# Optimization experiments

Hardware: AMD Instinct MI355X
Metric: run time of the kernel (lower is better)

The kernel has to match this reference:

```python
import jax, jax.numpy as jnp
import numpy as np

N = 50000        # nodes
E = 1_600_000    # edges
D_IN = 128       # input_dim
H = 2            # n_heads
C = 32           # out_dim per head


def setup_inputs() -> dict:
    key = jax.random.key(0)
    ks = jax.random.split(key, 10)
    x = jax.random.normal(ks[0], (N, D_IN), dtype=jnp.float32)
    edge_index = jax.random.randint(ks[1], (2, E), 0, N, dtype=jnp.int64)
    s = 1.0 / np.sqrt(D_IN)
    Wq = jax.random.uniform(ks[2], (D_IN, H * C), jnp.float32, -s, s)
    bq = jax.random.uniform(ks[3], (H * C,), jnp.float32, -s, s)
    Wk = jax.random.uniform(ks[4], (D_IN, H * C), jnp.float32, -s, s)
    bk = jax.random.uniform(ks[5], (H * C,), jnp.float32, -s, s)
    Wv = jax.random.uniform(ks[6], (D_IN, H * C), jnp.float32, -s, s)
    bv = jax.random.uniform(ks[7], (H * C,), jnp.float32, -s, s)
    Wskip = jax.random.uniform(ks[8], (D_IN, H * C), jnp.float32, -s, s)
    bskip = jax.random.uniform(ks[9], (H * C,), jnp.float32, -s, s)
    return {"x": x, "edge_index": edge_index, "Wq": Wq, "bq": bq,
            "Wk": Wk, "bk": bk, "Wv": Wv, "bv": bv,
            "Wskip": Wskip, "bskip": bskip}


def reference(x, edge_index, Wq, bq, Wk, bk, Wv, bv, Wskip, bskip):
    # IntraGraphAttention.forward: ELU then TransformerConv (PyG semantics,
    # concat=True, root_weight=True, beta=False).
    x = jax.nn.elu(x)
    src, dst = edge_index[0], edge_index[1]

    q = (x @ Wq + bq).reshape(N, H, C)   # queries at target nodes
    k = (x @ Wk + bk).reshape(N, H, C)   # keys at source nodes
    v = (x @ Wv + bv).reshape(N, H, C)   # values at source nodes

    # per-edge attention logits [E, H]
    alpha = jnp.einsum('ehc,ehc->eh', q[dst], k[src]) / np.sqrt(C).astype(np.float32)

    # segment softmax over incoming edges of each target node
    m = jax.ops.segment_max(alpha, dst, num_segments=N)            # [N, H]
    m = jnp.where(jnp.isfinite(m), m, 0.0)                          # empty segments
    ex = jnp.exp(alpha - m[dst])                                    # [E, H]
    denom = jax.ops.segment_sum(ex, dst, num_segments=N)            # [N, H]
    w = ex / jnp.maximum(denom[dst], 1e-16)                         # [E, H]

    # weighted scatter-add of values to targets
    msg = v[src] * w[:, :, None]                                    # [E, H, C]
    out = jax.ops.segment_sum(msg, dst, num_segments=N)             # [N, H, C]
    out = out.reshape(N, H * C)

    # root/skip connection
    return out + x @ Wskip + bskip
```

## Files before the change

kernel.cpp:

```cpp
#include <hip/hip_runtime.h>
#include <hip/hip_bf16.h>


#define DIN 128
#define HC  64
#define EPB 4096
#define CAPB 12288
#define CAPQ 3072

typedef _Float16 h2 __attribute__((ext_vector_type(2)));
typedef _Float16 h4 __attribute__((ext_vector_type(4)));
typedef _Float16 h8 __attribute__((ext_vector_type(8)));
typedef float    f4 __attribute__((ext_vector_type(4)));
typedef float    f2v __attribute__((ext_vector_type(2)));

#if defined(__has_builtin)
#if __has_builtin(__builtin_amdgcn_fdot2)
#define HAVE_FDOT2 1
#endif
#endif

static __device__ __forceinline__ float fdot2(h2 a, h2 b, float c) {
#ifdef HAVE_FDOT2
    return __builtin_amdgcn_fdot2(a, b, c, false);
#else
    return fmaf((float)a.x, (float)b.x, fmaf((float)a.y, (float)b.y, c));
#endif
}

__global__ __launch_bounds__(256) void k_prep(
        const float* __restrict__ Wq, const float* __restrict__ Wk,
        const float* __restrict__ Wv, const float* __restrict__ Ws,
        _Float16* __restrict__ Wh, int* __restrict__ bucketCnt) {
    int t = threadIdx.x;
    if (blockIdx.x == 0) bucketCnt[t] = 0;
    int idx = blockIdx.x * 256 + t;
    int m    = idx >> 13;
    int rem  = idx & 8191;
    int grp  = rem >> 9;
    int ks   = grp >> 2;
    int nt   = grp & 3;
    int r3   = rem & 511;
    int lane = r3 >> 3;
    int j    = r3 & 7;
    int k = ks * 32 + (lane >> 4) * 8 + j;
    int n = nt * 16 + (lane & 15);
    const float* W = (m == 0) ? Wq : (m == 1) ? Wk : (m == 2) ? Wv : Ws;
    Wh[idx] = (_Float16)W[k * 64 + n];
}

#define TB 32
#define XS 136
__global__ __launch_bounds__(256) void k_fused(
        const float4* __restrict__ x4,
        const _Float16* __restrict__ Wh,
        const float* __restrict__ bq, const float* __restrict__ bk,
        const float* __restrict__ bv, const float* __restrict__ bs,
        _Float16* __restrict__ Q, unsigned char* __restrict__ KV8,
        float* __restrict__ OUT, int N,
        const int* __restrict__ ei, int* __restrict__ bucketCnt,
        unsigned int* __restrict__ part, int E, int cb) {
    __shared__ alignas(16) char smem[4096 + EPB * 4];
    int t = threadIdx.x;

    if ((int)blockIdx.x < cb) {
        int* hist  = (int*)smem;
        int* lbase = hist + 256;
        int* gbase = lbase + 256;
        int* wsum  = gbase + 256;
        unsigned int* stg = (unsigned int*)(smem + 4096);

        int e0 = (int)blockIdx.x * EPB;
        int cnt = min(EPB, E - e0);
        hist[t] = 0;
        __syncthreads();

        unsigned int pk[EPB / 256];
        unsigned short rk[EPB / 256];
        #pragma unroll
        for (int u = 0; u < EPB / 256; ++u) {
            int i = t + u * 256;
            if (i < cnt) {
                unsigned int d = (unsigned int)ei[E + e0 + i];
                unsigned int s = (unsigned int)ei[e0 + i];
                pk[u] = (d << 16) | s;
                rk[u] = (unsigned short)atomicAdd(&hist[d >> 8], 1);
            }
        }
        __syncthreads();

        int lane = t & 63, wid = t >> 6;
        int v = hist[t];
        int x = v;
        #pragma unroll
        for (int off = 1; off < 64; off <<= 1) {
            int y = __shfl_up(x, off, 64);
            if (lane >= off) x += y;
        }
        if (lane == 63) wsum[wid] = x;
        __syncthreads();
        int wpre = 0;
        #pragma unroll
        for (int w = 0; w < 4; ++w) wpre += (w < wid) ? wsum[w] : 0;
        lbase[t] = wpre + x - v;
        if (v > 0) {
            int base = atomicAdd(&bucketCnt[t], v);
            base = min(base, CAPB - v);
            gbase[t] = t * CAPB + base;
        }
        __syncthreads();

        #pragma unroll
        for (int u = 0; u < EPB / 256; ++u) {
            int i = t + u * 256;
            if (i < cnt) stg[lbase[pk[u] >> 24] + (int)rk[u]] = pk[u];
        }
        __syncthreads();
        for (int i = t; i < cnt; i += 256) {
            unsigned int pkv = stg[i];
            int b = pkv >> 24;
            part[gbase[b] + (i - lbase[b])] = pkv;
        }
        return;
    }

    _Float16* xs = (_Float16*)smem;
    int n0 = ((int)blockIdx.x - cb) * TB;

    #pragma unroll
    for (int u = 0; u < 4; ++u) {
        int idx = t + u * 256;
        int row = idx >> 5;
        int k4  = idx & 31;
        int node = n0 + row;
        float4 v = make_float4(0.f, 0.f, 0.f, 0.f);
        if (node < N) v = x4[(size_t)node * 32 + k4];
        v.x = (v.x > 0.f) ? v.x : (__expf(v.x) - 1.0f);
        v.y = (v.y > 0.f) ? v.y : (__expf(v.y) - 1.0f);
        v.z = (v.z > 0.f) ? v.z : (__expf(v.z) - 1.0f);
        v.w = (v.w > 0.f) ? v.w : (__expf(v.w) - 1.0f);
        h4 hv = { (_Float16)v.x, (_Float16)v.y, (_Float16)v.z, (_Float16)v.w };
        *(h4*)&xs[row * XS + k4 * 4] = hv;
    }
    __syncthreads();

    int m    = t >> 6;
    int lane = t & 63;
    int lr   = lane & 15;
    int lq   = lane >> 4;

    const _Float16* Wm = Wh + m * 8192;
    const float* bias = (m == 0) ? bq : (m == 1) ? bk : (m == 2) ? bv : bs;

    f4 acc[2][4];
    #pragma unroll
    for (int mt = 0; mt < 2; ++mt)
        #pragma unroll
        for (int nt = 0; nt < 4; ++nt)
            acc[mt][nt] = (f4){0.f, 0.f, 0.f, 0.f};

    #pragma unroll
    for (int ks = 0; ks < 4; ++ks) {
        h8 a0 = *(const h8*)&xs[lr * XS + ks * 32 + lq * 8];
        h8 a1 = *(const h8*)&xs[(16 + lr) * XS + ks * 32 + lq * 8];
        #pragma unroll
        for (int nt = 0; nt < 4; ++nt) {
            h8 b = *(const h8*)&Wm[((ks * 4 + nt) << 9) + lane * 8];
            acc[0][nt] = __builtin_amdgcn_mfma_f32_16x16x32_f16(a0, b, acc[0][nt], 0, 0, 0);
            acc[1][nt] = __builtin_amdgcn_mfma_f32_16x16x32_f16(a1, b, acc[1][nt], 0, 0, 0);
        }
    }

    #pragma unroll
    for (int nt = 0; nt < 4; ++nt) {
        int col = nt * 16 + lr;
        float bb = bias[col];
        #pragma unroll
        for (int mt = 0; mt < 2; ++mt) {
            #pragma unroll
            for (int r = 0; r < 4; ++r) {
                int node = n0 + mt * 16 + lq * 4 + r;
                if (node < N) {
                    float val = acc[mt][nt][r] + bb;
                    if (m == 3) {
                        OUT[((size_t)node << 6) + col] = val;
                    } else if (m == 0) {
                        Q[((size_t)node << 6) + col] = (_Float16)val;
                    } else {
                        int pk8 = __builtin_amdgcn_cvt_pk_fp8_f32(val, val, 0, false);
                        KV8[((size_t)node << 7) + ((m == 2) ? 64 : 0) + col] =
                            (unsigned char)(pk8 & 0xFF);
                    }
                }
            }
        }
    }
}

__global__ __launch_bounds__(512) void k_build(
        const unsigned int* __restrict__ part, const int* __restrict__ bucketCnt,
        unsigned short* __restrict__ srcs16, int* __restrict__ row_ptr,
        int N, int NBK, int E) {
    __shared__ int hist[256], basep[256], cur[64], sd[256];
    __shared__ unsigned short sbuf[CAPQ];
    __shared__ int s_outBase, s_cnt;
    int t = threadIdx.x;
    int bqid = blockIdx.x;
    int b = bqid >> 2;
    int h = bqid & 3;

    int bc = (t < NBK) ? bucketCnt[t] : 0;
    if (t < 256) sd[t] = bc;
    __syncthreads();
    for (int off = 1; off < 256; off <<= 1) {
        int xv = (t >= off && t < 256) ? sd[t - off] : 0;
        __syncthreads();
        if (t < 256) sd[t] += xv;
        __syncthreads();
    }
    if (t == b) { s_outBase = sd[t] - bc; s_cnt = bc; }
    if (bqid == 0 && t == 256) row_ptr[N] = E;
    if (t < 256) hist[t] = 0;
    if (t < 64) cur[t] = 0;
    __syncthreads();
    int outBase = s_outBase;
    int cnt = min(s_cnt, CAPB);
    int s0 = b * CAPB;

    for (int i = t; i < cnt; i += 512) {
        atomicAdd(&hist[(part[s0 + i] >> 16) & 255], 1);
    }
    __syncthreads();
    {
        int v = (t < 256) ? hist[t] : 0;
        if (t < 256) sd[t] = v;
        __syncthreads();
        for (int off = 1; off < 256; off <<= 1) {
            int xv = (t >= off && t < 256) ? sd[t - off] : 0;
            __syncthreads();
            if (t < 256) sd[t] += xv;
            __syncthreads();
        }
        if (t < 256) basep[t] = sd[t] - v;
    }
    __syncthreads();

    int lo = h << 6;
    int base0 = basep[lo];
    int qcnt = ((h == 3) ? cnt : basep[lo + 64]) - base0;

    for (int i = t; i < cnt; i += 512) {
        unsigned int pkv = part[s0 + i];
        int d = (pkv >> 16) & 255;
        if ((d >> 6) == h) {
            int r = atomicAdd(&cur[d - lo], 1);
            int pos = basep[d] - base0 + r;
            if (pos < CAPQ) sbuf[pos] = (unsigned short)(pkv & 0xFFFFu);
        }
    }
    __syncthreads();
    for (int i = t; i < qcnt && i < CAPQ; i += 512)
        srcs16[outBase + base0 + i] = sbuf[i];

    int node = (b << 8) + lo + t;
    if (t < 64 && node < N) row_ptr[node] = outBase + basep[lo + t];
}

__global__ __launch_bounds__(256) void k_attn(
        const _Float16* __restrict__ Q, const unsigned char* __restrict__ KV8,
        const int* __restrict__ row_ptr,
        const unsigned short* __restrict__ srcs16, float* __restrict__ out, int N) {
    int lane = threadIdx.x & 63;
    int wave = threadIdx.x >> 6;
    int n = blockIdx.x * 4 + wave;
    if (n >= N) return;
    int h5 = lane & 32;
    int c  = lane & 31;
    int eg = (lane >> 3) & 3;
    int ch = lane & 7;

    int start = row_ptr[n];
    int deg   = row_ptr[n + 1] - start;
    if (deg <= 0) return;

    h8 q8[4];
    {
        const h8* qp = (const h8*)(Q + ((size_t)n << 6) + h5);
        #pragma unroll
        for (int r = 0; r < 4; ++r) q8[r] = qp[r];
    }
    const h2* q2 = (const h2*)q8;

    const float scale = 0.17677669529663687f;
    float lsum = 0.f;
    f4 acc = (f4){0.f, 0.f, 0.f, 0.f};

    unsigned vofs = 64u + (unsigned)h5 + ((unsigned)ch << 2);

    int sc_cur = (c < deg) ? (int)srcs16[start + c] : 0;
    uint4 ka, kb;
    {
        unsigned ko = ((unsigned)sc_cur << 7) + (unsigned)h5;
        ka = *(const uint4*)(KV8 + ko);
        kb = *(const uint4*)(KV8 + ko + 16);
    }

    for (int i0 = 0; i0 < deg; i0 += 32) {
        int nb = min(32, deg - i0);
        int sc = sc_cur;
        int i1 = i0 + 32;

        int sc_next = 0;
        if (i1 < deg && c < deg - i1) sc_next = (int)srcs16[start + i1 + c];

        float s0 = 0.f, s1 = 0.f, s2 = 0.f, s3 = 0.f;
#define KDOT(kw, idx, ss) { \
        f2v f01 = __builtin_amdgcn_cvt_pk_f32_fp8((int)(kw), false); \
        f2v f23 = __builtin_amdgcn_cvt_pk_f32_fp8((int)(kw), true);  \
        auto p01 = __builtin_amdgcn_cvt_pkrtz(f01[0], f01[1]); \
        auto p23 = __builtin_amdgcn_cvt_pkrtz(f23[0], f23[1]); \
        ss = fdot2(*(h2*)&p01, q2[2*(idx)],   ss); \
        ss = fdot2(*(h2*)&p23, q2[2*(idx)+1], ss); }
        KDOT(ka.x, 0, s0) KDOT(ka.y, 1, s1) KDOT(ka.z, 2, s2) KDOT(ka.w, 3, s3)
        KDOT(kb.x, 4, s0) KDOT(kb.y, 5, s1) KDOT(kb.z, 6, s2) KDOT(kb.w, 7, s3)
#undef KDOT
        float s = (s0 + s1) + (s2 + s3);
        float ex = (c < nb) ? __expf(s * scale) : 0.f;
        lsum += ex;

        if (i1 < deg) {
            unsigned ko = ((unsigned)sc_next << 7) + (unsigned)h5;
            ka = *(const uint4*)(KV8 + ko);
            kb = *(const uint4*)(KV8 + ko + 16);
        }
        sc_cur = sc_next;

        float wv[8]; int sj[8];
        #pragma unroll
        for (int u = 0; u < 8; ++u) {
            int j = 4 * u + eg;
            wv[u] = __shfl(ex, h5 + j, 64);
            sj[u] = __shfl(sc, h5 + j, 64);
        }
        unsigned vw[8];
        #pragma unroll
        for (int u = 0; u < 8; ++u)
            vw[u] = *(const unsigned int*)(KV8 + (((unsigned)sj[u] << 7) + vofs));
        #pragma unroll
        for (int u = 0; u < 8; ++u) {
            f2v v01 = __builtin_amdgcn_cvt_pk_f32_fp8((int)vw[u], false);
            f2v v23 = __builtin_amdgcn_cvt_pk_f32_fp8((int)vw[u], true);
            acc[0] = fmaf(wv[u], v01[0], acc[0]);
            acc[1] = fmaf(wv[u], v01[1], acc[1]);
            acc[2] = fmaf(wv[u], v23[0], acc[2]);
            acc[3] = fmaf(wv[u], v23[1], acc[3]);
        }
    }

    #pragma unroll
    for (int i = 0; i < 4; ++i) {
        acc[i] += __shfl_xor(acc[i], 8, 64);
        acc[i] += __shfl_xor(acc[i], 16, 64);
    }

    float ls = lsum;
    ls += __shfl_xor(ls, 16, 64);
    ls += __shfl_xor(ls,  8, 64);
    ls += __shfl_xor(ls,  4, 64);
    ls += __shfl_xor(ls,  2, 64);
    ls += __shfl_xor(ls,  1, 64);
    float rden = 1.0f / fmaxf(ls, 1e-16f);

    if ((lane & 24) == 0) {
        float4* o4 = (float4*)out + ((size_t)n << 4) + (h5 >> 2) + ch;
        float4 cur4 = *o4;
        cur4.x += acc[0] * rden;
        cur4.y += acc[1] * rden;
        cur4.z += acc[2] * rden;
        cur4.w += acc[3] * rden;
        *o4 = cur4;
    }
}

extern "C" void kernel_launch(void* const* d_in, const int* in_sizes, int n_in,
                              void* d_out, int out_size, void* d_ws, size_t ws_size,
                              hipStream_t stream) {
    const float* x  = (const float*)d_in[0];
    const int*   ei = (const int*)d_in[1];
    const float* Wq = (const float*)d_in[2];
    const float* bq = (const float*)d_in[3];
    const float* Wk = (const float*)d_in[4];
    const float* bk = (const float*)d_in[5];
    const float* Wv = (const float*)d_in[6];
    const float* bv = (const float*)d_in[7];
    const float* Ws = (const float*)d_in[8];
    const float* bs = (const float*)d_in[9];
    float* out = (float*)d_out;

    int N = in_sizes[0] / DIN;
    int E = in_sizes[1] / 2;
    int NBK = (N + 255) >> 8;

    char* ws = (char*)d_ws;
    size_t off = 0;
    auto carve = [&](size_t bytes) -> void* {
        void* p = ws + off;
        off = (off + bytes + 255) & ~(size_t)255;
        return p;
    };
    int*            bucketCnt = (int*)carve(256 * sizeof(int));
    int*            row_ptr   = (int*)carve((size_t)(N + 1) * sizeof(int));
    unsigned int*   part      = (unsigned int*)carve((size_t)NBK * CAPB * sizeof(unsigned int));
    unsigned short* srcs16    = (unsigned short*)carve((size_t)E * sizeof(unsigned short));
    _Float16*       Wh        = (_Float16*)carve(4 * 8192 * sizeof(_Float16));
    _Float16*       Qh        = (_Float16*)carve((size_t)N * HC * sizeof(_Float16));
    unsigned char*  KV8       = (unsigned char*)carve((size_t)N * 128);
    (void)ws_size; (void)n_in; (void)out_size;

    int qb = (N + TB - 1) / TB;
    int cb = (E + EPB - 1) / EPB;

    k_prep<<<128, 256, 0, stream>>>(Wq, Wk, Wv, Ws, Wh, bucketCnt);
    k_fused<<<qb + cb, 256, 0, stream>>>(
        (const float4*)x, Wh, bq, bk, bv, bs,
        Qh, KV8, out, N,
        ei, bucketCnt, part, E, cb);
    k_build<<<4 * NBK, 512, 0, stream>>>(part, bucketCnt, srcs16, row_ptr, N, NBK, E);
    k_attn<<<(N + 3) / 4, 256, 0, stream>>>(Qh, KV8, row_ptr, srcs16, out, N);
}
```

Before: 172.7 us.

## Replace bucketed two-pass CSR build with global degree histogram, scan, atomic scatter

Swaps the two-level radix partition (per-block LDS bucketing into a fixed-capacity staging buffer, then a per-bucket build kernel) for a counting-sort CSR build. A global per-node degree histogram is built with atomics, a two-kernel prefix scan produces row_ptr and cursors, and a scatter pass places each source via a global atomicAdd on its destination cursor. This drops the capacity-clamped partition buffer and the build kernel. In exchange it adds a memset, two extra launches, an extra read of the edge list, and 1.6M contended global atomics with random 2-byte writes. Neighbor order within a row becomes nondeterministic.

```diff
diff --git a/kernel.cpp b/kernel.cpp
--- a/kernel.cpp
+++ b/kernel.cpp
@@ -4,9 +4,6 @@
 
 #define DIN 128
 #define HC  64
-#define EPB 4096
-#define CAPB 12288
-#define CAPQ 3072
 
 typedef _Float16 h2 __attribute__((ext_vector_type(2)));
 typedef _Float16 h4 __attribute__((ext_vector_type(4)));
@@ -31,22 +28,80 @@
 __global__ __launch_bounds__(256) void k_prep(
         const float* __restrict__ Wq, const float* __restrict__ Wk,
         const float* __restrict__ Wv, const float* __restrict__ Ws,
-        _Float16* __restrict__ Wh, int* __restrict__ bucketCnt) {
+        _Float16* __restrict__ Wh,
+        const int* __restrict__ ei, int* __restrict__ deg, int E) {
     int t = threadIdx.x;
-    if (blockIdx.x == 0) bucketCnt[t] = 0;
-    int idx = blockIdx.x * 256 + t;
-    int m    = idx >> 13;
-    int rem  = idx & 8191;
-    int grp  = rem >> 9;
-    int ks   = grp >> 2;
-    int nt   = grp & 3;
-    int r3   = rem & 511;
-    int lane = r3 >> 3;
-    int j    = r3 & 7;
-    int k = ks * 32 + (lane >> 4) * 8 + j;
-    int n = nt * 16 + (lane & 15);
-    const float* W = (m == 0) ? Wq : (m == 1) ? Wk : (m == 2) ? Wv : Ws;
-    Wh[idx] = (_Float16)W[k * 64 + n];
+    if ((int)blockIdx.x < 128) {
+        int idx = blockIdx.x * 256 + t;
+        int m    = idx >> 13;
+        int rem  = idx & 8191;
+        int grp  = rem >> 9;
+        int ks   = grp >> 2;
+        int nt   = grp & 3;
+        int r3   = rem & 511;
+        int lane = r3 >> 3;
+        int j    = r3 & 7;
+        int k = ks * 32 + (lane >> 4) * 8 + j;
+        int n = nt * 16 + (lane & 15);
+        const float* W = (m == 0) ? Wq : (m == 1) ? Wk : (m == 2) ? Wv : Ws;
+        Wh[idx] = (_Float16)W[k * 64 + n];
+        return;
+    }
+    int base = ((int)blockIdx.x - 128) * 1024;
+    #pragma unroll
+    for (int u = 0; u < 4; ++u) {
+        int i = base + u * 256 + t;
+        if (i < E) atomicAdd(&deg[ei[E + i]], 1);
+    }
+}
+
+__global__ __launch_bounds__(256) void k_scanA(
+        const int* __restrict__ deg, int* __restrict__ chunkSum, int N) {
+    int t = threadIdx.x;
+    int node = (int)blockIdx.x * 256 + t;
+    int v = (node < N) ? deg[node] : 0;
+    #pragma unroll
+    for (int off = 1; off < 64; off <<= 1) v += __shfl_xor(v, off, 64);
+    __shared__ int ws[4];
+    if ((t & 63) == 0) ws[t >> 6] = v;
+    __syncthreads();
+    if (t == 0) chunkSum[blockIdx.x] = ws[0] + ws[1] + ws[2] + ws[3];
+}
+
+__global__ __launch_bounds__(256) void k_scanB(
+        const int* __restrict__ deg, const int* __restrict__ chunkSum,
+        int* __restrict__ row_ptr, int* __restrict__ cur, int N, int E) {
+    __shared__ int ws[4], sbase[1];
+    int t = threadIdx.x, j = (int)blockIdx.x;
+    int lane = t & 63, wid = t >> 6;
+
+    int c = (t < j) ? chunkSum[t] : 0;
+    int cr = c;
+    #pragma unroll
+    for (int off = 1; off < 64; off <<= 1) cr += __shfl_xor(cr, off, 64);
+    if (lane == 0) ws[wid] = cr;
+    __syncthreads();
+    if (t == 0) sbase[0] = ws[0] + ws[1] + ws[2] + ws[3];
+    __syncthreads();
+    int base = sbase[0];
+    __syncthreads();
+
+    int node = j * 256 + t;
+    int v = (node < N) ? deg[node] : 0;
+    int x = v;
+    #pragma unroll
+    for (int off = 1; off < 64; off <<= 1) {
+        int y = __shfl_up(x, off, 64);
+        if (lane >= off) x += y;
+    }
+    if (lane == 63) ws[wid] = x;
+    __syncthreads();
+    int wpre = 0;
+    #pragma unroll
+    for (int w = 0; w < 4; ++w) wpre += (w < wid) ? ws[w] : 0;
+    int excl = base + wpre + x - v;
+    if (node < N) { row_ptr[node] = excl; cur[node] = excl; }
+    if (j == 0 && t == 0) row_ptr[N] = E;
 }
 
 #define TB 32
@@ -58,74 +113,27 @@
         const float* __restrict__ bv, const float* __restrict__ bs,
         _Float16* __restrict__ Q, unsigned char* __restrict__ KV8,
         float* __restrict__ OUT, int N,
-        const int* __restrict__ ei, int* __restrict__ bucketCnt,
-        unsigned int* __restrict__ part, int E, int cb) {
-    __shared__ alignas(16) char smem[4096 + EPB * 4];
+        const int* __restrict__ ei, int* __restrict__ cur,
+        unsigned short* __restrict__ srcs16, int E, int qb) {
+    __shared__ alignas(16) _Float16 xs[32 * XS];
     int t = threadIdx.x;
 
-    if ((int)blockIdx.x < cb) {
-        int* hist  = (int*)smem;
-        int* lbase = hist + 256;
-        int* gbase = lbase + 256;
-        int* wsum  = gbase + 256;
-        unsigned int* stg = (unsigned int*)(smem + 4096);
-
-        int e0 = (int)blockIdx.x * EPB;
-        int cnt = min(EPB, E - e0);
-        hist[t] = 0;
-        __syncthreads();
-
-        unsigned int pk[EPB / 256];
-        unsigned short rk[EPB / 256];
-        #pragma unroll
-        for (int u = 0; u < EPB / 256; ++u) {
-            int i = t + u * 256;
-            if (i < cnt) {
-                unsigned int d = (unsigned int)ei[E + e0 + i];
-                unsigned int s = (unsigned int)ei[e0 + i];
-                pk[u] = (d << 16) | s;
-                rk[u] = (unsigned short)atomicAdd(&hist[d >> 8], 1);
+    if ((int)blockIdx.x >= qb) {
+        int base = ((int)blockIdx.x - qb) * 1024;
+        #pragma unroll
+        for (int u = 0; u < 4; ++u) {
+            int i = base + u * 256 + t;
+            if (i < E) {
+                int s = ei[i];
+                int d = ei[E + i];
+                int pos = atomicAdd(&cur[d], 1);
+                srcs16[pos] = (unsigned short)s;
             }
         }
-        __syncthreads();
-
-        int lane = t & 63, wid = t >> 6;
-        int v = hist[t];
-        int x = v;
-        #pragma unroll
-        for (int off = 1; off < 64; off <<= 1) {
-            int y = __shfl_up(x, off, 64);
-            if (lane >= off) x += y;
-        }
-        if (lane == 63) wsum[wid] = x;
-        __syncthreads();
-        int wpre = 0;
-        #pragma unroll
-        for (int w = 0; w < 4; ++w) wpre += (w < wid) ? wsum[w] : 0;
-        lbase[t] = wpre + x - v;
-        if (v > 0) {
-            int base = atomicAdd(&bucketCnt[t], v);
-            base = min(base, CAPB - v);
-            gbase[t] = t * CAPB + base;
-        }
-        __syncthreads();
-
-        #pragma unroll
-        for (int u = 0; u < EPB / 256; ++u) {
-            int i = t + u * 256;
-            if (i < cnt) stg[lbase[pk[u] >> 24] + (int)rk[u]] = pk[u];
-        }
-        __syncthreads();
-        for (int i = t; i < cnt; i += 256) {
-            unsigned int pkv = stg[i];
-            int b = pkv >> 24;
-            part[gbase[b] + (i - lbase[b])] = pkv;
-        }
         return;
     }
 
-    _Float16* xs = (_Float16*)smem;
-    int n0 = ((int)blockIdx.x - cb) * TB;
+    int n0 = (int)blockIdx.x * TB;
 
     #pragma unroll
     for (int u = 0; u < 4; ++u) {
@@ -197,75 +205,6 @@
     }
 }
 
-__global__ __launch_bounds__(512) void k_build(
-        const unsigned int* __restrict__ part, const int* __restrict__ bucketCnt,
-        unsigned short* __restrict__ srcs16, int* __restrict__ row_ptr,
-        int N, int NBK, int E) {
-    __shared__ int hist[256], basep[256], cur[64], sd[256];
-    __shared__ unsigned short sbuf[CAPQ];
-    __shared__ int s_outBase, s_cnt;
-    int t = threadIdx.x;
-    int bqid = blockIdx.x;
-    int b = bqid >> 2;
-    int h = bqid & 3;
-
-    int bc = (t < NBK) ? bucketCnt[t] : 0;
-    if (t < 256) sd[t] = bc;
-    __syncthreads();
-    for (int off = 1; off < 256; off <<= 1) {
-        int xv = (t >= off && t < 256) ? sd[t - off] : 0;
-        __syncthreads();
-        if (t < 256) sd[t] += xv;
-        __syncthreads();
-    }
-    if (t == b) { s_outBase = sd[t] - bc; s_cnt = bc; }
-    if (bqid == 0 && t == 256) row_ptr[N] = E;
-    if (t < 256) hist[t] = 0;
-    if (t < 64) cur[t] = 0;
-    __syncthreads();
-    int outBase = s_outBase;
-    int cnt = min(s_cnt, CAPB);
-    int s0 = b * CAPB;
-
-    for (int i = t; i < cnt; i += 512) {
-        atomicAdd(&hist[(part[s0 + i] >> 16) & 255], 1);
-    }
-    __syncthreads();
-    {
-        int v = (t < 256) ? hist[t] : 0;
-        if (t < 256) sd[t] = v;
-        __syncthreads();
-        for (int off = 1; off < 256; off <<= 1) {
-            int xv = (t >= off && t < 256) ? sd[t - off] : 0;
-            __syncthreads();
-            if (t < 256) sd[t] += xv;
-            __syncthreads();
-        }
-        if (t < 256) basep[t] = sd[t] - v;
-    }
-    __syncthreads();
-
-    int lo = h << 6;
-    int base0 = basep[lo];
-    int qcnt = ((h == 3) ? cnt : basep[lo + 64]) - base0;
-
-    for (int i = t; i < cnt; i += 512) {
-        unsigned int pkv = part[s0 + i];
-        int d = (pkv >> 16) & 255;
-        if ((d >> 6) == h) {
-            int r = atomicAdd(&cur[d - lo], 1);
-            int pos = basep[d] - base0 + r;
-            if (pos < CAPQ) sbuf[pos] = (unsigned short)(pkv & 0xFFFFu);
-        }
-    }
-    __syncthreads();
-    for (int i = t; i < qcnt && i < CAPQ; i += 512)
-        srcs16[outBase + base0 + i] = sbuf[i];
-
-    int node = (b << 8) + lo + t;
-    if (t < 64 && node < N) row_ptr[node] = outBase + basep[lo + t];
-}
-
 __global__ __launch_bounds__(256) void k_attn(
         const _Float16* __restrict__ Q, const unsigned char* __restrict__ KV8,
         const int* __restrict__ row_ptr,
@@ -408,9 +347,10 @@
         off = (off + bytes + 255) & ~(size_t)255;
         return p;
     };
-    int*            bucketCnt = (int*)carve(256 * sizeof(int));
+    int*            deg       = (int*)carve((size_t)N * sizeof(int));
+    int*            cur       = (int*)carve((size_t)N * sizeof(int));
     int*            row_ptr   = (int*)carve((size_t)(N + 1) * sizeof(int));
-    unsigned int*   part      = (unsigned int*)carve((size_t)NBK * CAPB * sizeof(unsigned int));
+    int*            chunkSum  = (int*)carve((size_t)NBK * sizeof(int));
     unsigned short* srcs16    = (unsigned short*)carve((size_t)E * sizeof(unsigned short));
     _Float16*       Wh        = (_Float16*)carve(4 * 8192 * sizeof(_Float16));
     _Float16*       Qh        = (_Float16*)carve((size_t)N * HC * sizeof(_Float16));
@@ -418,13 +358,15 @@
     (void)ws_size; (void)n_in; (void)out_size;
 
     int qb = (N + TB - 1) / TB;
-    int cb = (E + EPB - 1) / EPB;
-
-    k_prep<<<128, 256, 0, stream>>>(Wq, Wk, Wv, Ws, Wh, bucketCnt);
-    k_fused<<<qb + cb, 256, 0, stream>>>(
+    int eb = (E + 1023) / 1024;
+
+    hipMemsetAsync(deg, 0, (size_t)N * sizeof(int), stream);
+    k_prep<<<128 + eb, 256, 0, stream>>>(Wq, Wk, Wv, Ws, Wh, ei, deg, E);
+    k_scanA<<<NBK, 256, 0, stream>>>(deg, chunkSum, N);
+    k_scanB<<<NBK, 256, 0, stream>>>(deg, chunkSum, row_ptr, cur, N, E);
+    k_fused<<<qb + eb, 256, 0, stream>>>(
         (const float4*)x, Wh, bq, bk, bv, bs,
         Qh, KV8, out, N,
-        ei, bucketCnt, part, E, cb);
-    k_build<<<4 * NBK, 512, 0, stream>>>(part, bucketCnt, srcs16, row_ptr, N, NBK, E);
+        ei, cur, srcs16, E, qb);
     k_attn<<<(N + 3) / 4, 256, 0, stream>>>(Qh, KV8, row_ptr, srcs16, out, N);
 }
```

After: 344.3 us. +99.3%, slower.

## Rewrite CSR build as one 1024-thread block per bucket with register-held ranks

Applied to the files above, without the earlier changes.

The CSR build kernel now runs one 1024-thread block per 256-node bucket instead of four 512-thread blocks per bucket that each handled a quarter of the destinations. Each thread reads its partition entries once into registers, takes its local rank from the histogram atomic, and scatters using the exclusive scan, so the second global read and the per-quarter cursor atomics are gone. Both scans use wave shuffles instead of a barrier-heavy shared-memory loop. The cost is fewer blocks in flight, a larger shared buffer and more registers per thread, which may limit occupancy.

```diff
diff --git a/kernel.cpp b/kernel.cpp
--- a/kernel.cpp
+++ b/kernel.cpp
@@ -6,7 +6,6 @@
 #define HC  64
 #define EPB 4096
 #define CAPB 12288
-#define CAPQ 3072
 
 typedef _Float16 h2 __attribute__((ext_vector_type(2)));
 typedef _Float16 h4 __attribute__((ext_vector_type(4)));
@@ -197,73 +196,82 @@
     }
 }
 
-__global__ __launch_bounds__(512) void k_build(
+__global__ __launch_bounds__(1024) void k_build(
         const unsigned int* __restrict__ part, const int* __restrict__ bucketCnt,
         unsigned short* __restrict__ srcs16, int* __restrict__ row_ptr,
         int N, int NBK, int E) {
-    __shared__ int hist[256], basep[256], cur[64], sd[256];
-    __shared__ unsigned short sbuf[CAPQ];
+    __shared__ int hist[256], basep[256], wsum[4], sums[4];
+    __shared__ unsigned short sbuf[CAPB];
     __shared__ int s_outBase, s_cnt;
     int t = threadIdx.x;
-    int bqid = blockIdx.x;
-    int b = bqid >> 2;
-    int h = bqid & 3;
-
-    int bc = (t < NBK) ? bucketCnt[t] : 0;
-    if (t < 256) sd[t] = bc;
-    __syncthreads();
-    for (int off = 1; off < 256; off <<= 1) {
-        int xv = (t >= off && t < 256) ? sd[t - off] : 0;
-        __syncthreads();
-        if (t < 256) sd[t] += xv;
-        __syncthreads();
-    }
-    if (t == b) { s_outBase = sd[t] - bc; s_cnt = bc; }
-    if (bqid == 0 && t == 256) row_ptr[N] = E;
-    if (t < 256) hist[t] = 0;
-    if (t < 64) cur[t] = 0;
-    __syncthreads();
+    int b = blockIdx.x;
+    int lane = t & 63, wid = t >> 6;
+
+    if (t < 256) {
+        hist[t] = 0;
+        int c = (t < NBK && t < b) ? bucketCnt[t] : 0;
+        #pragma unroll
+        for (int off = 1; off < 64; off <<= 1) c += __shfl_xor(c, off, 64);
+        if (lane == 0) sums[wid] = c;
+    }
+    if (t == 1023) s_cnt = min(bucketCnt[b], CAPB);
+    __syncthreads();
+    if (t == 0) s_outBase = sums[0] + sums[1] + sums[2] + sums[3];
+    __syncthreads();
+    int cnt = s_cnt;
     int outBase = s_outBase;
-    int cnt = min(s_cnt, CAPB);
     int s0 = b * CAPB;
 
-    for (int i = t; i < cnt; i += 512) {
-        atomicAdd(&hist[(part[s0 + i] >> 16) & 255], 1);
-    }
-    __syncthreads();
-    {
-        int v = (t < 256) ? hist[t] : 0;
-        if (t < 256) sd[t] = v;
-        __syncthreads();
-        for (int off = 1; off < 256; off <<= 1) {
-            int xv = (t >= off && t < 256) ? sd[t - off] : 0;
-            __syncthreads();
-            if (t < 256) sd[t] += xv;
-            __syncthreads();
-        }
-        if (t < 256) basep[t] = sd[t] - v;
-    }
-    __syncthreads();
-
-    int lo = h << 6;
-    int base0 = basep[lo];
-    int qcnt = ((h == 3) ? cnt : basep[lo + 64]) - base0;
-
-    for (int i = t; i < cnt; i += 512) {
-        unsigned int pkv = part[s0 + i];
-        int d = (pkv >> 16) & 255;
-        if ((d >> 6) == h) {
-            int r = atomicAdd(&cur[d - lo], 1);
-            int pos = basep[d] - base0 + r;
-            if (pos < CAPQ) sbuf[pos] = (unsigned short)(pkv & 0xFFFFu);
-        }
-    }
-    __syncthreads();
-    for (int i = t; i < qcnt && i < CAPQ; i += 512)
-        srcs16[outBase + base0 + i] = sbuf[i];
-
-    int node = (b << 8) + lo + t;
-    if (t < 64 && node < N) row_ptr[node] = outBase + basep[lo + t];
+    unsigned int pk[CAPB / 1024];
+    int rk[CAPB / 1024];
+    #pragma unroll
+    for (int u = 0; u < CAPB / 1024; ++u) {
+        int i = t + u * 1024;
+        if (i < cnt) {
+            pk[u] = part[s0 + i];
+            rk[u] = atomicAdd(&hist[(pk[u] >> 16) & 255], 1);
+        }
+    }
+    __syncthreads();
+
+    if (t < 256) {
+        int v = hist[t];
+        int x = v;
+        #pragma unroll
+        for (int off = 1; off < 64; off <<= 1) {
+            int y = __shfl_up(x, off, 64);
+            if (lane >= off) x += y;
+        }
+        if (lane == 63) wsum[wid] = x;
+        basep[t] = x - v;
+    }
+    __syncthreads();
+    if (t < 256) {
+        int wpre = 0;
+        #pragma unroll
+        for (int w = 0; w < 4; ++w) wpre += (w < wid) ? wsum[w] : 0;
+        basep[t] += wpre;
+    }
+    __syncthreads();
+
+    #pragma unroll
+    for (int u = 0; u < CAPB / 1024; ++u) {
+        int i = t + u * 1024;
+        if (i < cnt) {
+            int d = (pk[u] >> 16) & 255;
+            int pos = basep[d] + rk[u];
+            if (pos < CAPB) sbuf[pos] = (unsigned short)(pk[u] & 0xFFFFu);
+        }
+    }
+    __syncthreads();
+
+    for (int i = t; i < cnt; i += 1024)
+        srcs16[outBase + i] = sbuf[i];
+    if (t < 256) {
+        int node = (b << 8) + t;
+        if (node < N) row_ptr[node] = outBase + basep[t];
+    }
+    if (b == 0 && t == 1023) row_ptr[N] = E;
 }
 
 __global__ __launch_bounds__(256) void k_attn(
@@ -425,6 +433,6 @@
         (const float4*)x, Wh, bq, bk, bv, bs,
         Qh, KV8, out, N,
         ei, bucketCnt, part, E, cb);
-    k_build<<<4 * NBK, 512, 0, stream>>>(part, bucketCnt, srcs16, row_ptr, N, NBK, E);
+    k_build<<<NBK, 1024, 0, stream>>>(part, bucketCnt, srcs16, row_ptr, N, NBK, E);
     k_attn<<<(N + 3) / 4, 256, 0, stream>>>(Qh, KV8, row_ptr, srcs16, out, N);
 }
```

Result: faster. 165.4 us (-4.2%).
